# Kernel tuning notes

Measured on AMD Instinct MI355X. Metric: run time of the kernel, lower is better.

## Reference

```python
import jax, jax.numpy as jnp
import numpy as np

N_EMBED = 384
HEAD = 64
BLOCK = 8
BATCH = 32768


def setup_inputs() -> dict:
    key = jax.random.key(0)
    kx, kq, kk, kv = jax.random.split(key, 4)
    x = jax.random.normal(kx, (BATCH, BLOCK, N_EMBED), dtype=jnp.float32)
    # torch nn.Linear(n_embed, head, bias=False): weight [head, n_embed], y = x @ W.T.
    # Store transposed [n_embed, head] so the reference uses a plain matmul.
    s = 1.0 / np.sqrt(N_EMBED)
    Wq = jax.random.uniform(kq, (N_EMBED, HEAD), jnp.float32, -s, s)
    Wk = jax.random.uniform(kk, (N_EMBED, HEAD), jnp.float32, -s, s)
    Wv = jax.random.uniform(kv, (N_EMBED, HEAD), jnp.float32, -s, s)
    return {"x": x, "Wq": Wq, "Wk": Wk, "Wv": Wv}


def reference(x, Wq, Wk, Wv):
    B, T, C = x.shape
    q = x @ Wq                      # [B, T, H]
    k = x @ Wk                      # [B, T, H]
    v = x @ Wv                      # [B, T, H]
    # NOTE: original scales by C**-0.5 where C = n_embed (not head dim) — keep faithful.
    scale = jnp.asarray(C, x.dtype) ** -0.5
    wei = jnp.einsum('bth,bsh->bts', q, k) * scale   # [B, T, T]
    mask = jnp.tril(jnp.ones((T, T), dtype=bool))
    wei = jnp.where(mask, wei, jnp.asarray(-jnp.inf, wei.dtype))
    wei = jax.nn.softmax(wei, axis=-1)
    # dropout is identity in eval mode
    return jnp.einsum('bts,bsh->bth', wei, v)        # [B, T, H]
```

## Files before the change

### kernel.cpp

```cpp
#include <hip/hip_runtime.h>
#include <hip/hip_bf16.h>

#define NE 384
#define HD 64
#define TT 8
#define NBATCH 32768

typedef __bf16 bf16;
typedef bf16 bf16x8 __attribute__((ext_vector_type(8)));
typedef bf16 bf16x4 __attribute__((ext_vector_type(4)));
typedef float f32x4 __attribute__((ext_vector_type(4)));

#define GLOAD_LDS16(g, l) __builtin_amdgcn_global_load_lds(                    \
    (const __attribute__((address_space(1))) void*)(g),                        \
    (__attribute__((address_space(3))) void*)(l), 16, 0, 0)

__global__ void prep_wt(const float* __restrict__ Wq, const float* __restrict__ Wk,
                        const float* __restrict__ Wv, bf16* __restrict__ wt) {
    int c = blockIdx.x * blockDim.x + threadIdx.x;
    if (c >= 12 * 12 * 64) return;
    int kk   = c / (12 * 64);
    int rem  = c % (12 * 64);
    int n    = rem / 64;
    int lane = rem % 64;
    int col  = n * 16 + (lane & 15);
    const float* src; int cc;
    if (col < 64)       { src = Wq; cc = col; }
    else if (col < 128) { src = Wk; cc = col - 64; }
    else                { src = Wv; cc = col - 128; }
    int k0 = kk * 32 + (lane >> 4) * 8;
    bf16* dst = wt + (size_t)c * 8;
    #pragma unroll
    for (int j = 0; j < 8; ++j)
        dst[j] = (bf16)src[(size_t)(k0 + j) * 64 + cc];
}

template<bool PREP>
__global__ __launch_bounds__(256, 3)
void fused_head(const float* __restrict__ x, const bf16* __restrict__ wt,
                const float* __restrict__ Wq, const float* __restrict__ Wk,
                const float* __restrict__ Wv, float* __restrict__ out) {
    constexpr int STQ = 72;
    constexpr int STV = 40;
    constexpr int WSZ = 2 * 16 * STQ + 64 * STV + 16 * STV;
    constexpr int BBUF = 12 * 512;
    __shared__ __align__(16) bf16 smem[4 * WSZ];

    const int tid  = threadIdx.x;
    const int wid  = tid >> 6;
    const int lane = tid & 63;
    const int lr   = lane & 15;
    const int lg   = lane >> 4;

    bf16* q2  = smem + wid * WSZ;
    bf16* k2  = q2 + 16 * STQ;
    bf16* vT  = k2 + 16 * STQ;
    bf16* wei = vT + 64 * STV;

    const int wg   = blockIdx.x * 4 + wid;
    const int row0 = wg * 32;

    f32x4 acc[2][12];
    #pragma unroll
    for (int m = 0; m < 2; ++m)
        #pragma unroll
        for (int n = 0; n < 12; ++n) acc[m][n] = f32x4{0.f, 0.f, 0.f, 0.f};

    const float* xb0 = x + (size_t)(row0 + lr) * NE + lg * 8;
    const float* xb1 = xb0 + (size_t)16 * NE;

    f32x4 c0lo = __builtin_nontemporal_load((const f32x4*)(xb0));
    f32x4 c0hi = __builtin_nontemporal_load((const f32x4*)(xb0 + 4));
    f32x4 c1lo = __builtin_nontemporal_load((const f32x4*)(xb1));
    f32x4 c1hi = __builtin_nontemporal_load((const f32x4*)(xb1 + 4));

    if (PREP) {
        #pragma unroll
        for (int i = 0; i < 3; ++i) {
            int n = wid * 3 + i;
            GLOAD_LDS16(wt + ((size_t)(0 * 12 + n) * 64 + lane) * 8,
                        smem + n * 512);
        }
        __syncthreads();

        for (int kk = 0; kk < 12; ++kk) {
            const int cur = kk & 1;
            if (kk < 11) {
                #pragma unroll
                for (int i = 0; i < 3; ++i) {
                    int n = wid * 3 + i;
                    GLOAD_LDS16(wt + ((size_t)((kk + 1) * 12 + n) * 64 + lane) * 8,
                                smem + (cur ^ 1) * BBUF + n * 512);
                }
            }

            bf16x8 a0, a1;
            #pragma unroll
            for (int j = 0; j < 4; ++j) {
                a0[j]     = (bf16)c0lo[j];
                a0[j + 4] = (bf16)c0hi[j];
                a1[j]     = (bf16)c1lo[j];
                a1[j + 4] = (bf16)c1hi[j];
            }

            if (kk < 11) {
                const float* p0 = xb0 + (kk + 1) * 32;
                const float* p1 = xb1 + (kk + 1) * 32;
                c0lo = __builtin_nontemporal_load((const f32x4*)(p0));
                c0hi = __builtin_nontemporal_load((const f32x4*)(p0 + 4));
                c1lo = __builtin_nontemporal_load((const f32x4*)(p1));
                c1hi = __builtin_nontemporal_load((const f32x4*)(p1 + 4));
            }

            const bf16* bb = smem + cur * BBUF;
            #pragma unroll
            for (int n = 0; n < 12; ++n) {
                bf16x8 b = *(const bf16x8*)(bb + n * 512 + lane * 8);
                acc[0][n] = __builtin_amdgcn_mfma_f32_16x16x32_bf16(a0, b, acc[0][n], 0, 0, 0);
                acc[1][n] = __builtin_amdgcn_mfma_f32_16x16x32_bf16(a1, b, acc[1][n], 0, 0, 0);
            }
            __syncthreads();
        }
    } else {
        for (int kk = 0; kk < 12; ++kk) {
            bf16x8 a0, a1;
            #pragma unroll
            for (int j = 0; j < 4; ++j) {
                a0[j]     = (bf16)c0lo[j];
                a0[j + 4] = (bf16)c0hi[j];
                a1[j]     = (bf16)c1lo[j];
                a1[j + 4] = (bf16)c1hi[j];
            }
            if (kk < 11) {
                const float* p0 = xb0 + (kk + 1) * 32;
                const float* p1 = xb1 + (kk + 1) * 32;
                c0lo = *(const f32x4*)(p0);
                c0hi = *(const f32x4*)(p0 + 4);
                c1lo = *(const f32x4*)(p1);
                c1hi = *(const f32x4*)(p1 + 4);
            }
            #pragma unroll
            for (int n = 0; n < 12; ++n) {
                int col = n * 16 + lr;
                const float* ws = (col < 64) ? (Wq + col)
                                 : (col < 128) ? (Wk + (col - 64))
                                               : (Wv + (col - 128));
                bf16x8 b;
                #pragma unroll
                for (int j = 0; j < 8; ++j)
                    b[j] = (bf16)ws[(size_t)(kk * 32 + lg * 8 + j) * 64];
                acc[0][n] = __builtin_amdgcn_mfma_f32_16x16x32_bf16(a0, b, acc[0][n], 0, 0, 0);
                acc[1][n] = __builtin_amdgcn_mfma_f32_16x16x32_bf16(a1, b, acc[1][n], 0, 0, 0);
            }
        }
    }

    {
        unsigned int* z = (unsigned int*)(vT + lane * STV + 16);
        #pragma unroll
        for (int j = 0; j < 8; ++j) z[j] = 0u;
        if (lane < 16) {
            unsigned int* zw = (unsigned int*)(wei + lane * STV + 16);
            #pragma unroll
            for (int j = 0; j < 8; ++j) zw[j] = 0u;
        }
    }

    const float qk_scale = 0.051031036307982884f;
    const f32x4 zero4 = {0.f, 0.f, 0.f, 0.f};

    #pragma unroll
    for (int p = 0; p < 2; ++p) {
        #pragma unroll
        for (int nt = 0; nt < 4; ++nt) {
            #pragma unroll
            for (int r = 0; r < 4; ++r) {
                q2[(4 * lg + r) * STQ + nt * 16 + lr] = (bf16)acc[p][nt][r];
                k2[(4 * lg + r) * STQ + nt * 16 + lr] = (bf16)acc[p][4 + nt][r];
            }
            bf16x4 vv;
            vv[0] = (bf16)acc[p][8 + nt][0];
            vv[1] = (bf16)acc[p][8 + nt][1];
            vv[2] = (bf16)acc[p][8 + nt][2];
            vv[3] = (bf16)acc[p][8 + nt][3];
            *(bf16x4*)(vT + (nt * 16 + lr) * STV + lg * 4) = vv;
        }

        f32x4 w4 = zero4;
        #pragma unroll
        for (int kh = 0; kh < 2; ++kh) {
            bf16x8 qa = *(const bf16x8*)(q2 + lr * STQ + kh * 32 + lg * 8);
            bf16x8 kb = *(const bf16x8*)(k2 + lr * STQ + kh * 32 + lg * 8);
            w4 = __builtin_amdgcn_mfma_f32_16x16x32_bf16(qa, kb, w4, 0, 0, 0);
        }

        const int sb = lr >> 3;
        const int s  = lr & 7;
        #pragma unroll
        for (int r = 0; r < 4; ++r) {
            int tp = 4 * lg + r;
            bool valid = ((tp >> 3) == sb) && (s <= (tp & 7));
            float val = valid ? w4[r] * qk_scale : -1e30f;
            float mx = val;
            mx = fmaxf(mx, __shfl_xor(mx, 1));
            mx = fmaxf(mx, __shfl_xor(mx, 2));
            mx = fmaxf(mx, __shfl_xor(mx, 4));
            float e = valid ? __expf(val - mx) : 0.f;
            float sm = e;
            sm += __shfl_xor(sm, 1);
            sm += __shfl_xor(sm, 2);
            sm += __shfl_xor(sm, 4);
            float pn = valid ? e / sm : 0.f;
            wei[tp * STV + lr] = (bf16)pn;
        }

        bf16x8 pa = *(const bf16x8*)(wei + lr * STV + lg * 8);
        const int bb2 = wg * 4 + p * 2;
        #pragma unroll
        for (int nt = 0; nt < 4; ++nt) {
            bf16x8 vb = *(const bf16x8*)(vT + (nt * 16 + lr) * STV + lg * 8);
            f32x4 o = __builtin_amdgcn_mfma_f32_16x16x32_bf16(pa, vb, zero4, 0, 0, 0);
            #pragma unroll
            for (int r = 0; r < 4; ++r) {
                int tp = 4 * lg + r;
                __builtin_nontemporal_store(o[r],
                    &out[((size_t)(bb2 + (tp >> 3)) * TT + (tp & 7)) * HD + nt * 16 + lr]);
            }
        }
    }
}

extern "C" void kernel_launch(void* const* d_in, const int* in_sizes, int n_in,
                              void* d_out, int out_size, void* d_ws, size_t ws_size,
                              hipStream_t stream) {
    const float* x  = (const float*)d_in[0];
    const float* Wq = (const float*)d_in[1];
    const float* Wk = (const float*)d_in[2];
    const float* Wv = (const float*)d_in[3];
    float* out = (float*)d_out;

    const size_t wt_bytes = (size_t)12 * 12 * 64 * 8 * sizeof(bf16);
    const int grid = NBATCH / 16;

    if (ws_size >= wt_bytes) {
        bf16* wt = (bf16*)d_ws;
        prep_wt<<<36, 256, 0, stream>>>(Wq, Wk, Wv, wt);
        fused_head<true><<<grid, 256, 0, stream>>>(x, wt, nullptr, nullptr, nullptr, out);
    } else {
        fused_head<false><<<grid, 256, 0, stream>>>(x, nullptr, Wq, Wk, Wv, out);
    }
}
```

Measured before the change: 124.8 us.

## Stage full bf16 weight matrix in LDS once per 512-thread block

Each block now grows to 8 waves and loads the entire 144 KB bf16 QKV weight tile into LDS up front, replacing the per-k-step double-buffered weight streaming and its barrier. The goal is to remove the 12 per-iteration __syncthreads and amortize weight loads across twice as many waves. The x-row prefetch is also deepened from one to three k-steps in registers. In exchange, LDS use per block rises sharply (likely one block per CU), which may reduce occupancy and latency hiding. The per-wave attention scratch now reuses the weight region after a barrier.

```diff
diff --git a/kernel.cpp b/kernel.cpp
--- a/kernel.cpp
+++ b/kernel.cpp
@@ -36,15 +36,14 @@
 }
 
 template<bool PREP>
-__global__ __launch_bounds__(256, 3)
+__global__ __launch_bounds__(512, 2)
 void fused_head(const float* __restrict__ x, const bf16* __restrict__ wt,
                 const float* __restrict__ Wq, const float* __restrict__ Wk,
                 const float* __restrict__ Wv, float* __restrict__ out) {
     constexpr int STQ = 72;
     constexpr int STV = 40;
     constexpr int WSZ = 2 * 16 * STQ + 64 * STV + 16 * STV;
-    constexpr int BBUF = 12 * 512;
-    __shared__ __align__(16) bf16 smem[4 * WSZ];
+    __shared__ __align__(16) bf16 smem[73728];
 
     const int tid  = threadIdx.x;
     const int wid  = tid >> 6;
@@ -52,12 +51,7 @@
     const int lr   = lane & 15;
     const int lg   = lane >> 4;
 
-    bf16* q2  = smem + wid * WSZ;
-    bf16* k2  = q2 + 16 * STQ;
-    bf16* vT  = k2 + 16 * STQ;
-    bf16* wei = vT + 64 * STV;
-
-    const int wg   = blockIdx.x * 4 + wid;
+    const int wg   = blockIdx.x * 8 + wid;
     const int row0 = wg * 32;
 
     f32x4 acc[2][12];
@@ -69,75 +63,71 @@
     const float* xb0 = x + (size_t)(row0 + lr) * NE + lg * 8;
     const float* xb1 = xb0 + (size_t)16 * NE;
 
-    f32x4 c0lo = __builtin_nontemporal_load((const f32x4*)(xb0));
-    f32x4 c0hi = __builtin_nontemporal_load((const f32x4*)(xb0 + 4));
-    f32x4 c1lo = __builtin_nontemporal_load((const f32x4*)(xb1));
-    f32x4 c1hi = __builtin_nontemporal_load((const f32x4*)(xb1 + 4));
+    f32x4 ab[3][4];
+    #pragma unroll
+    for (int s = 0; s < 3; ++s) {
+        const float* p0 = xb0 + s * 32;
+        const float* p1 = xb1 + s * 32;
+        ab[s][0] = __builtin_nontemporal_load((const f32x4*)(p0));
+        ab[s][1] = __builtin_nontemporal_load((const f32x4*)(p0 + 4));
+        ab[s][2] = __builtin_nontemporal_load((const f32x4*)(p1));
+        ab[s][3] = __builtin_nontemporal_load((const f32x4*)(p1 + 4));
+    }
 
     if (PREP) {
         #pragma unroll
-        for (int i = 0; i < 3; ++i) {
-            int n = wid * 3 + i;
-            GLOAD_LDS16(wt + ((size_t)(0 * 12 + n) * 64 + lane) * 8,
-                        smem + n * 512);
+        for (int r = 0; r < 18; ++r) {
+            int c = wid * 18 + r;
+            GLOAD_LDS16(wt + ((size_t)c * 64 + lane) * 8, smem + c * 512);
         }
         __syncthreads();
 
+        #pragma unroll
         for (int kk = 0; kk < 12; ++kk) {
-            const int cur = kk & 1;
-            if (kk < 11) {
-                #pragma unroll
-                for (int i = 0; i < 3; ++i) {
-                    int n = wid * 3 + i;
-                    GLOAD_LDS16(wt + ((size_t)((kk + 1) * 12 + n) * 64 + lane) * 8,
-                                smem + (cur ^ 1) * BBUF + n * 512);
-                }
-            }
-
+            const int slot = kk % 3;
             bf16x8 a0, a1;
             #pragma unroll
             for (int j = 0; j < 4; ++j) {
-                a0[j]     = (bf16)c0lo[j];
-                a0[j + 4] = (bf16)c0hi[j];
-                a1[j]     = (bf16)c1lo[j];
-                a1[j + 4] = (bf16)c1hi[j];
-            }
-
-            if (kk < 11) {
-                const float* p0 = xb0 + (kk + 1) * 32;
-                const float* p1 = xb1 + (kk + 1) * 32;
-                c0lo = __builtin_nontemporal_load((const f32x4*)(p0));
-                c0hi = __builtin_nontemporal_load((const f32x4*)(p0 + 4));
-                c1lo = __builtin_nontemporal_load((const f32x4*)(p1));
-                c1hi = __builtin_nontemporal_load((const f32x4*)(p1 + 4));
-            }
-
-            const bf16* bb = smem + cur * BBUF;
+                a0[j]     = (bf16)ab[slot][0][j];
+                a0[j + 4] = (bf16)ab[slot][1][j];
+                a1[j]     = (bf16)ab[slot][2][j];
+                a1[j + 4] = (bf16)ab[slot][3][j];
+            }
+            if (kk + 3 < 12) {
+                const float* p0 = xb0 + (kk + 3) * 32;
+                const float* p1 = xb1 + (kk + 3) * 32;
+                ab[slot][0] = __builtin_nontemporal_load((const f32x4*)(p0));
+                ab[slot][1] = __builtin_nontemporal_load((const f32x4*)(p0 + 4));
+                ab[slot][2] = __builtin_nontemporal_load((const f32x4*)(p1));
+                ab[slot][3] = __builtin_nontemporal_load((const f32x4*)(p1 + 4));
+            }
             #pragma unroll
             for (int n = 0; n < 12; ++n) {
-                bf16x8 b = *(const bf16x8*)(bb + n * 512 + lane * 8);
+                bf16x8 b = *(const bf16x8*)(smem + ((kk * 12 + n) * 64 + lane) * 8);
                 acc[0][n] = __builtin_amdgcn_mfma_f32_16x16x32_bf16(a0, b, acc[0][n], 0, 0, 0);
                 acc[1][n] = __builtin_amdgcn_mfma_f32_16x16x32_bf16(a1, b, acc[1][n], 0, 0, 0);
             }
-            __syncthreads();
-        }
+        }
+        __syncthreads();
     } else {
+        #pragma unroll
         for (int kk = 0; kk < 12; ++kk) {
+            const int slot = kk % 3;
             bf16x8 a0, a1;
             #pragma unroll
             for (int j = 0; j < 4; ++j) {
-                a0[j]     = (bf16)c0lo[j];
-                a0[j + 4] = (bf16)c0hi[j];
-                a1[j]     = (bf16)c1lo[j];
-                a1[j + 4] = (bf16)c1hi[j];
-            }
-            if (kk < 11) {
-                const float* p0 = xb0 + (kk + 1) * 32;
-                const float* p1 = xb1 + (kk + 1) * 32;
-                c0lo = *(const f32x4*)(p0);
-                c0hi = *(const f32x4*)(p0 + 4);
-                c1lo = *(const f32x4*)(p1);
-                c1hi = *(const f32x4*)(p1 + 4);
+                a0[j]     = (bf16)ab[slot][0][j];
+                a0[j + 4] = (bf16)ab[slot][1][j];
+                a1[j]     = (bf16)ab[slot][2][j];
+                a1[j + 4] = (bf16)ab[slot][3][j];
+            }
+            if (kk + 3 < 12) {
+                const float* p0 = xb0 + (kk + 3) * 32;
+                const float* p1 = xb1 + (kk + 3) * 32;
+                ab[slot][0] = *(const f32x4*)(p0);
+                ab[slot][1] = *(const f32x4*)(p0 + 4);
+                ab[slot][2] = *(const f32x4*)(p1);
+                ab[slot][3] = *(const f32x4*)(p1 + 4);
             }
             #pragma unroll
             for (int n = 0; n < 12; ++n) {
@@ -153,7 +143,13 @@
                 acc[1][n] = __builtin_amdgcn_mfma_f32_16x16x32_bf16(a1, b, acc[1][n], 0, 0, 0);
             }
         }
-    }
+        __syncthreads();
+    }
+
+    bf16* q2  = smem + wid * WSZ;
+    bf16* k2  = q2 + 16 * STQ;
+    bf16* vT  = k2 + 16 * STQ;
+    bf16* wei = vT + 64 * STV;
 
     {
         unsigned int* z = (unsigned int*)(vT + lane * STV + 16);
@@ -240,13 +236,13 @@
     float* out = (float*)d_out;
 
     const size_t wt_bytes = (size_t)12 * 12 * 64 * 8 * sizeof(bf16);
-    const int grid = NBATCH / 16;
+    const int grid = NBATCH / 32;
 
     if (ws_size >= wt_bytes) {
         bf16* wt = (bf16*)d_ws;
         prep_wt<<<36, 256, 0, stream>>>(Wq, Wk, Wv, wt);
-        fused_head<true><<<grid, 256, 0, stream>>>(x, wt, nullptr, nullptr, nullptr, out);
+        fused_head<true><<<grid, 512, 0, stream>>>(x, wt, nullptr, nullptr, nullptr, out);
     } else {
-        fused_head<false><<<grid, 256, 0, stream>>>(x, nullptr, Wq, Wk, Wv, out);
+        fused_head<false><<<grid, 512, 0, stream>>>(x, nullptr, Wq, Wk, Wv, out);
     }
 }
```

Measured after the change: 122.6 us. About the same (-1.8%).

## Alias per-wave LDS scratch regions and raise occupancy target to five blocks

Applied to the files above, without the earlier changes.

Shrinks each wave's LDS scratch so that q/k and vT/wei alias the same region, with explicit lgkmcnt fences between the phases, and raises launch_bounds min blocks from 3 to 5 to allow more resident workgroups per CU. The zero padding is rewritten every pass because of the aliasing. Nontemporal loads and stores of x and out become ordinary accesses. The higher occupancy target may force register spills of the 24 accumulator vectors, and the aliasing depends on the fences being correct.

```diff
diff --git a/kernel.cpp b/kernel.cpp
--- a/kernel.cpp
+++ b/kernel.cpp
@@ -14,6 +14,8 @@
 #define GLOAD_LDS16(g, l) __builtin_amdgcn_global_load_lds(                    \
     (const __attribute__((address_space(1))) void*)(g),                        \
     (__attribute__((address_space(3))) void*)(l), 16, 0, 0)
+
+#define LDS_FENCE() asm volatile("s_waitcnt lgkmcnt(0)" ::: "memory")
 
 __global__ void prep_wt(const float* __restrict__ Wq, const float* __restrict__ Wk,
                         const float* __restrict__ Wv, bf16* __restrict__ wt) {
@@ -36,13 +38,13 @@
 }
 
 template<bool PREP>
-__global__ __launch_bounds__(256, 3)
+__global__ __launch_bounds__(256, 5)
 void fused_head(const float* __restrict__ x, const bf16* __restrict__ wt,
                 const float* __restrict__ Wq, const float* __restrict__ Wk,
                 const float* __restrict__ Wv, float* __restrict__ out) {
     constexpr int STQ = 72;
     constexpr int STV = 40;
-    constexpr int WSZ = 2 * 16 * STQ + 64 * STV + 16 * STV;
+    constexpr int WSZ = 3200;
     constexpr int BBUF = 12 * 512;
     __shared__ __align__(16) bf16 smem[4 * WSZ];
 
@@ -52,10 +54,11 @@
     const int lr   = lane & 15;
     const int lg   = lane >> 4;
 
-    bf16* q2  = smem + wid * WSZ;
-    bf16* k2  = q2 + 16 * STQ;
-    bf16* vT  = k2 + 16 * STQ;
-    bf16* wei = vT + 64 * STV;
+    bf16* base = smem + wid * WSZ;
+    bf16* q2  = base;
+    bf16* k2  = base + 16 * STQ;
+    bf16* vT  = base;
+    bf16* wei = base + 64 * STV;
 
     const int wg   = blockIdx.x * 4 + wid;
     const int row0 = wg * 32;
@@ -69,10 +72,10 @@
     const float* xb0 = x + (size_t)(row0 + lr) * NE + lg * 8;
     const float* xb1 = xb0 + (size_t)16 * NE;
 
-    f32x4 c0lo = __builtin_nontemporal_load((const f32x4*)(xb0));
-    f32x4 c0hi = __builtin_nontemporal_load((const f32x4*)(xb0 + 4));
-    f32x4 c1lo = __builtin_nontemporal_load((const f32x4*)(xb1));
-    f32x4 c1hi = __builtin_nontemporal_load((const f32x4*)(xb1 + 4));
+    f32x4 c0lo = *(const f32x4*)(xb0);
+    f32x4 c0hi = *(const f32x4*)(xb0 + 4);
+    f32x4 c1lo = *(const f32x4*)(xb1);
+    f32x4 c1hi = *(const f32x4*)(xb1 + 4);
 
     if (PREP) {
         #pragma unroll
@@ -106,10 +109,10 @@
             if (kk < 11) {
                 const float* p0 = xb0 + (kk + 1) * 32;
                 const float* p1 = xb1 + (kk + 1) * 32;
-                c0lo = __builtin_nontemporal_load((const f32x4*)(p0));
-                c0hi = __builtin_nontemporal_load((const f32x4*)(p0 + 4));
-                c1lo = __builtin_nontemporal_load((const f32x4*)(p1));
-                c1hi = __builtin_nontemporal_load((const f32x4*)(p1 + 4));
+                c0lo = *(const f32x4*)(p0);
+                c0hi = *(const f32x4*)(p0 + 4);
+                c1lo = *(const f32x4*)(p1);
+                c1hi = *(const f32x4*)(p1 + 4);
             }
 
             const bf16* bb = smem + cur * BBUF;
@@ -153,24 +156,19 @@
                 acc[1][n] = __builtin_amdgcn_mfma_f32_16x16x32_bf16(a1, b, acc[1][n], 0, 0, 0);
             }
         }
-    }
-
-    {
-        unsigned int* z = (unsigned int*)(vT + lane * STV + 16);
-        #pragma unroll
-        for (int j = 0; j < 8; ++j) z[j] = 0u;
-        if (lane < 16) {
-            unsigned int* zw = (unsigned int*)(wei + lane * STV + 16);
-            #pragma unroll
-            for (int j = 0; j < 8; ++j) zw[j] = 0u;
-        }
+        __syncthreads();
     }
 
     const float qk_scale = 0.051031036307982884f;
     const f32x4 zero4 = {0.f, 0.f, 0.f, 0.f};
+    bf16x8 bzero;
+    #pragma unroll
+    for (int j = 0; j < 8; ++j) bzero[j] = (bf16)0.f;
 
     #pragma unroll
     for (int p = 0; p < 2; ++p) {
+        LDS_FENCE();
+
         #pragma unroll
         for (int nt = 0; nt < 4; ++nt) {
             #pragma unroll
@@ -178,24 +176,19 @@
                 q2[(4 * lg + r) * STQ + nt * 16 + lr] = (bf16)acc[p][nt][r];
                 k2[(4 * lg + r) * STQ + nt * 16 + lr] = (bf16)acc[p][4 + nt][r];
             }
-            bf16x4 vv;
-            vv[0] = (bf16)acc[p][8 + nt][0];
-            vv[1] = (bf16)acc[p][8 + nt][1];
-            vv[2] = (bf16)acc[p][8 + nt][2];
-            vv[3] = (bf16)acc[p][8 + nt][3];
-            *(bf16x4*)(vT + (nt * 16 + lr) * STV + lg * 4) = vv;
-        }
+        }
+        bf16x8 qa0 = *(const bf16x8*)(q2 + lr * STQ + 0 * 32 + lg * 8);
+        bf16x8 kb0 = *(const bf16x8*)(k2 + lr * STQ + 0 * 32 + lg * 8);
+        bf16x8 qa1 = *(const bf16x8*)(q2 + lr * STQ + 1 * 32 + lg * 8);
+        bf16x8 kb1 = *(const bf16x8*)(k2 + lr * STQ + 1 * 32 + lg * 8);
 
         f32x4 w4 = zero4;
-        #pragma unroll
-        for (int kh = 0; kh < 2; ++kh) {
-            bf16x8 qa = *(const bf16x8*)(q2 + lr * STQ + kh * 32 + lg * 8);
-            bf16x8 kb = *(const bf16x8*)(k2 + lr * STQ + kh * 32 + lg * 8);
-            w4 = __builtin_amdgcn_mfma_f32_16x16x32_bf16(qa, kb, w4, 0, 0, 0);
-        }
+        w4 = __builtin_amdgcn_mfma_f32_16x16x32_bf16(qa0, kb0, w4, 0, 0, 0);
+        w4 = __builtin_amdgcn_mfma_f32_16x16x32_bf16(qa1, kb1, w4, 0, 0, 0);
 
         const int sb = lr >> 3;
         const int s  = lr & 7;
+        float pn[4];
         #pragma unroll
         for (int r = 0; r < 4; ++r) {
             int tp = 4 * lg + r;
@@ -210,9 +203,30 @@
             sm += __shfl_xor(sm, 1);
             sm += __shfl_xor(sm, 2);
             sm += __shfl_xor(sm, 4);
-            float pn = valid ? e / sm : 0.f;
-            wei[tp * STV + lr] = (bf16)pn;
-        }
+            pn[r] = valid ? e / sm : 0.f;
+        }
+
+        LDS_FENCE();
+
+        *(bf16x8*)(vT + lane * STV + 16) = bzero;
+        *(bf16x8*)(vT + lane * STV + 24) = bzero;
+        if (lane < 16) {
+            *(bf16x8*)(wei + lane * STV + 16) = bzero;
+            *(bf16x8*)(wei + lane * STV + 24) = bzero;
+        }
+
+        #pragma unroll
+        for (int nt = 0; nt < 4; ++nt) {
+            bf16x4 vv;
+            vv[0] = (bf16)acc[p][8 + nt][0];
+            vv[1] = (bf16)acc[p][8 + nt][1];
+            vv[2] = (bf16)acc[p][8 + nt][2];
+            vv[3] = (bf16)acc[p][8 + nt][3];
+            *(bf16x4*)(vT + (nt * 16 + lr) * STV + lg * 4) = vv;
+        }
+        #pragma unroll
+        for (int r = 0; r < 4; ++r)
+            wei[(4 * lg + r) * STV + lr] = (bf16)pn[r];
 
         bf16x8 pa = *(const bf16x8*)(wei + lr * STV + lg * 8);
         const int bb2 = wg * 4 + p * 2;
@@ -223,8 +237,7 @@
             #pragma unroll
             for (int r = 0; r < 4; ++r) {
                 int tp = 4 * lg + r;
-                __builtin_nontemporal_store(o[r],
-                    &out[((size_t)(bb2 + (tp >> 3)) * TT + (tp & 7)) * HD + nt * 16 + lr]);
+                out[((size_t)(bb2 + (tp >> 3)) * TT + (tp & 7)) * HD + nt * 16 + lr] = o[r];
             }
         }
     }
```

New measurement: 324.7 us. 160% more time.
